# Performance work log

Hardware: AMD Instinct MI355X
Metric: run time of the kernel (lower is better)

Reference implementation:

```python
import jax, jax.numpy as jnp
import numpy as np
from jax import lax

B, C, H, W = 32, 256, 64, 64
BN_EPS = 1e-5
GRN_EPS = 1e-6


def _dwconv(x, w):
    # x: (B,C,H,W), w: (C,1,k,k) depthwise (feature_group_count=C), 'same' padding
    k = w.shape[-1]
    p = k // 2
    return lax.conv_general_dilated(
        x, w, window_strides=(1, 1), padding=[(p, p), (p, p)],
        feature_group_count=x.shape[1],
        dimension_numbers=('NCHW', 'OIHW', 'NCHW'))


def _bn(x, w, b, m, v):
    # eval-mode BatchNorm2d, per-channel affine
    scale = (w * lax.rsqrt(v + BN_EPS))[None, :, None, None]
    shift = (b - m * w * lax.rsqrt(v + BN_EPS))[None, :, None, None]
    return x * scale + shift


def setup_inputs() -> dict:
    key = jax.random.key(0)
    ks = jax.random.split(key, 6)
    ones = jnp.ones((C,), jnp.float32)
    zeros = jnp.zeros((C,), jnp.float32)
    return {
        'x': jax.random.normal(ks[0], (B, C, H, W), jnp.float32),
        'dw_w3': jax.random.normal(ks[1], (C, 1, 3, 3), jnp.float32) * 0.1,
        'bn3_w': ones, 'bn3_b': zeros, 'bn3_m': zeros, 'bn3_v': ones,
        'dw_w5': jax.random.normal(ks[2], (C, 1, 5, 5), jnp.float32) * 0.1,
        'bn5_w': ones, 'bn5_b': zeros, 'bn5_m': zeros, 'bn5_v': ones,
        'dw_w7': jax.random.normal(ks[3], (C, 1, 7, 7), jnp.float32) * 0.1,
        'bn7_w': ones, 'bn7_b': zeros, 'bn7_m': zeros, 'bn7_v': ones,
        'pw_w': jax.random.normal(ks[4], (C, C), jnp.float32) * (1.0 / np.sqrt(C)),
        'pwbn_w': ones, 'pwbn_b': zeros, 'pwbn_m': zeros, 'pwbn_v': ones,
        'grn_gamma': zeros, 'grn_beta': zeros,
    }


def reference(x, dw_w3, bn3_w, bn3_b, bn3_m, bn3_v,
              dw_w5, bn5_w, bn5_b, bn5_m, bn5_v,
              dw_w7, bn7_w, bn7_b, bn7_m, bn7_v,
              pw_w, pwbn_w, pwbn_b, pwbn_m, pwbn_v,
              grn_gamma, grn_beta):
    residual = x
    gelu = lambda t: jax.nn.gelu(t, approximate=False)  # torch nn.GELU default (erf)
    out = gelu(_bn(_dwconv(x, dw_w3), bn3_w, bn3_b, bn3_m, bn3_v))
    out = out + gelu(_bn(_dwconv(x, dw_w5), bn5_w, bn5_b, bn5_m, bn5_v))
    out = out + gelu(_bn(_dwconv(x, dw_w7), bn7_w, bn7_b, bn7_m, bn7_v))
    out = out / 3.0
    # pointwise 1x1 conv: contraction over channel dim
    out = jnp.einsum('bchw,oc->bohw', out, pw_w)
    out = _bn(out, pwbn_w, pwbn_b, pwbn_m, pwbn_v)
    # GRN: L2 norm over spatial dims per (B,C)
    Gx = jnp.sqrt(jnp.sum(out * out, axis=(2, 3), keepdims=True))  # (B,C,1,1)
    Nx = Gx / (jnp.mean(Gx, axis=1, keepdims=True) + GRN_EPS)
    out = out + grn_gamma[None, :, None, None] * (out * Nx) + grn_beta[None, :, None, None]
    out = out + residual
    return gelu(out)
```

## Files before the change

### kernel.cpp

```cpp
#include <hip/hip_runtime.h>
#include <hip/hip_bf16.h>
#include <math.h>

#define BB 32
#define CC 256
#define HH 64
#define HW 4096

typedef __attribute__((ext_vector_type(8))) short short8;
typedef __attribute__((ext_vector_type(4))) float f32x4;

__device__ __forceinline__ float gelu_erf(float x) {
    return 0.5f * x * (1.0f + erff(x * 0.70710678118654752f));
}

__global__ __launch_bounds__(256) void k_prep(const float* __restrict__ pw,
                                              __hip_bfloat16* __restrict__ pwb)
{
    const int i = blockIdx.x * 256 + threadIdx.x;
    pwb[i] = __float2bfloat16(pw[i]);
}

__global__ __launch_bounds__(256) void k_dwconv(
    const float* __restrict__ x,
    const float* __restrict__ w3,
    const float* __restrict__ bn3w, const float* __restrict__ bn3b,
    const float* __restrict__ bn3m, const float* __restrict__ bn3v,
    const float* __restrict__ w5,
    const float* __restrict__ bn5w, const float* __restrict__ bn5b,
    const float* __restrict__ bn5m, const float* __restrict__ bn5v,
    const float* __restrict__ w7,
    const float* __restrict__ bn7w, const float* __restrict__ bn7b,
    const float* __restrict__ bn7m, const float* __restrict__ bn7v,
    __hip_bfloat16* __restrict__ mid)
{
    __shared__ float sm[70 * 70];
    __shared__ float wl[83];
    __shared__ float bnp[6];
    const int tid = threadIdx.x;
    const int blk = blockIdx.x;
    const int c = blk & 255;
    const int b = blk >> 8;
    const float* xp = x + ((size_t)(b * CC + c)) * HW;

    for (int i = tid; i < 4900; i += 256) {
        int r = i / 70, q = i - r * 70;
        int h = r - 3, w = q - 3;
        float v = 0.f;
        if ((unsigned)h < 64u && (unsigned)w < 64u) v = xp[h * 64 + w];
        sm[i] = v;
    }
    if (tid < 9) wl[tid] = w3[c * 9 + tid];
    else if (tid < 34) wl[tid] = w5[c * 25 + tid - 9];
    else if (tid < 83) wl[tid] = w7[c * 49 + tid - 34];
    else if (tid == 83) {
        float s = bn3w[c] * rsqrtf(bn3v[c] + 1e-5f);
        bnp[0] = s; bnp[1] = bn3b[c] - bn3m[c] * s;
    } else if (tid == 84) {
        float s = bn5w[c] * rsqrtf(bn5v[c] + 1e-5f);
        bnp[2] = s; bnp[3] = bn5b[c] - bn5m[c] * s;
    } else if (tid == 85) {
        float s = bn7w[c] * rsqrtf(bn7v[c] + 1e-5f);
        bnp[4] = s; bnp[5] = bn7b[c] - bn7m[c] * s;
    }
    __syncthreads();

    const int ti = tid >> 4, tj = tid & 15;
    float a3[16], a5[16], a7[16];
#pragma unroll
    for (int i = 0; i < 16; ++i) { a3[i] = 0.f; a5[i] = 0.f; a7[i] = 0.f; }
    const float* w3l = wl;
    const float* w5l = wl + 9;
    const float* w7l = wl + 34;

#pragma unroll
    for (int pr = 0; pr < 10; ++pr) {
        float r[10];
        const float* srow = &sm[(ti * 4 + pr) * 70 + tj * 4];
#pragma unroll
        for (int q = 0; q < 10; ++q) r[q] = srow[q];
#pragma unroll
        for (int i = 0; i < 4; ++i) {
            const int k7 = pr - i;
            if (k7 >= 0 && k7 <= 6) {
#pragma unroll
                for (int j = 0; j < 4; ++j) {
                    float s = 0.f;
#pragma unroll
                    for (int dx = 0; dx < 7; ++dx) s += r[j + dx] * w7l[k7 * 7 + dx];
                    a7[i * 4 + j] += s;
                }
            }
            const int k5 = pr - 1 - i;
            if (k5 >= 0 && k5 <= 4) {
#pragma unroll
                for (int j = 0; j < 4; ++j) {
                    float s = 0.f;
#pragma unroll
                    for (int dx = 0; dx < 5; ++dx) s += r[j + dx + 1] * w5l[k5 * 5 + dx];
                    a5[i * 4 + j] += s;
                }
            }
            const int k3 = pr - 2 - i;
            if (k3 >= 0 && k3 <= 2) {
#pragma unroll
                for (int j = 0; j < 4; ++j) {
                    float s = 0.f;
#pragma unroll
                    for (int dx = 0; dx < 3; ++dx) s += r[j + dx + 2] * w3l[k3 * 3 + dx];
                    a3[i * 4 + j] += s;
                }
            }
        }
    }

    const float s3 = bnp[0], h3 = bnp[1], s5 = bnp[2], h5 = bnp[3], s7 = bnp[4], h7 = bnp[5];
    __hip_bfloat16* mp = mid + ((size_t)(b * CC + c)) * HW;
#pragma unroll
    for (int i = 0; i < 4; ++i) {
        __hip_bfloat16 o[4];
#pragma unroll
        for (int j = 0; j < 4; ++j) {
            float v = gelu_erf(a3[i * 4 + j] * s3 + h3)
                    + gelu_erf(a5[i * 4 + j] * s5 + h5)
                    + gelu_erf(a7[i * 4 + j] * s7 + h7);
            o[j] = __float2bfloat16(v * (1.0f / 3.0f));
        }
        *(uint2*)&mp[(ti * 4 + i) * 64 + tj * 4] = *(uint2*)o;
    }
}

#define ASTR 68
#define BSTR 40
__global__ __launch_bounds__(256) void k_pw(
    const __hip_bfloat16* __restrict__ mid,
    const __hip_bfloat16* __restrict__ pwb,
    const float* __restrict__ pbw, const float* __restrict__ pbb,
    const float* __restrict__ pbm, const float* __restrict__ pbv,
    __hip_bfloat16* __restrict__ out2,
    float* __restrict__ gx2)
{
    __shared__ __align__(16) short As[32 * ASTR];
    __shared__ __align__(16) short Bs[256 * BSTR];
    __shared__ float sc[256], sh[256], gxp[256];

    const int tid = threadIdx.x;
    const int blk = blockIdx.x;
    const int mt = blk & 63, b = blk >> 6;
    const int hw0 = mt * 64;

    {
        float s = pbw[tid] * rsqrtf(pbv[tid] + 1e-5f);
        sc[tid] = s;
        sh[tid] = pbb[tid] - pbm[tid] * s;
        gxp[tid] = 0.f;
    }

    const int wv = tid >> 6, lane = tid & 63;
    const int qd = lane >> 4, ln16 = lane & 15;

    f32x4 acc[16];
#pragma unroll
    for (int i = 0; i < 16; ++i) acc[i] = (f32x4){0.f, 0.f, 0.f, 0.f};

    const int ak = tid >> 3, am = tid & 7;
    const __hip_bfloat16* aptr = mid + ((size_t)(b * CC + ak)) * HW + hw0 + am * 8;
    const __hip_bfloat16* bptr = pwb + (size_t)tid * 256;

    for (int kk = 0; kk < 8; ++kk) {
        __syncthreads();
        uint4 av = *(const uint4*)(aptr + (size_t)kk * 32 * HW);
        *(uint2*)&As[ak * ASTR + am * 8]     = make_uint2(av.x, av.y);
        *(uint2*)&As[ak * ASTR + am * 8 + 4] = make_uint2(av.z, av.w);
        const uint4* bp = (const uint4*)(bptr + kk * 32);
#pragma unroll
        for (int j = 0; j < 4; ++j) {
            *(uint4*)&Bs[tid * BSTR + j * 8] = bp[j];
        }
        __syncthreads();

        short8 af;
        const int mloc = wv * 16 + ln16;
#pragma unroll
        for (int j = 0; j < 8; ++j) af[j] = As[(qd * 8 + j) * ASTR + mloc];
#pragma unroll
        for (int nt = 0; nt < 16; ++nt) {
            short8 bf = *(short8*)&Bs[(nt * 16 + ln16) * BSTR + qd * 8];
            acc[nt] = __builtin_amdgcn_mfma_f32_16x16x32_bf16(af, bf, acc[nt], 0, 0, 0);
        }
    }

    const size_t obase = ((size_t)b * CC) * HW + hw0 + wv * 16 + qd * 4;
#pragma unroll
    for (int nt = 0; nt < 16; ++nt) {
        const int o = nt * 16 + ln16;
        const float s = sc[o], h = sh[o];
        float v0 = acc[nt][0] * s + h;
        float v1 = acc[nt][1] * s + h;
        float v2 = acc[nt][2] * s + h;
        float v3 = acc[nt][3] * s + h;
        float p = v0 * v0 + v1 * v1 + v2 * v2 + v3 * v3;
        p += __shfl_xor(p, 16);
        p += __shfl_xor(p, 32);
        if ((lane & 48) == 0) atomicAdd(&gxp[o], p);
        __hip_bfloat16 ov[4];
        ov[0] = __float2bfloat16(v0);
        ov[1] = __float2bfloat16(v1);
        ov[2] = __float2bfloat16(v2);
        ov[3] = __float2bfloat16(v3);
        *(uint2*)&out2[obase + (size_t)o * HW] = *(uint2*)ov;
    }
    __syncthreads();
    atomicAdd(&gx2[b * CC + tid], gxp[tid]);
}

__global__ __launch_bounds__(256) void k_grn(const float* __restrict__ gx2,
                                             float* __restrict__ nx)
{
    const int b = blockIdx.x, t = threadIdx.x;
    const float g = sqrtf(gx2[b * 256 + t]);
    float s = g;
#pragma unroll
    for (int m = 1; m <= 32; m <<= 1) s += __shfl_xor(s, m);
    __shared__ float ws4[4];
    if ((t & 63) == 0) ws4[t >> 6] = s;
    __syncthreads();
    const float tot = ws4[0] + ws4[1] + ws4[2] + ws4[3];
    const float mean = tot * (1.0f / 256.0f);
    nx[b * 256 + t] = g / (mean + 1e-6f);
}

__global__ __launch_bounds__(256) void k_final(
    const __hip_bfloat16* __restrict__ out2,
    const float* __restrict__ x,
    const float* __restrict__ gamma,
    const float* __restrict__ beta,
    const float* __restrict__ nx,
    float* __restrict__ out)
{
    const size_t e = ((size_t)blockIdx.x * 256 + threadIdx.x) * 8;
    const int bc = (int)(e >> 12);
    const int c = bc & 255;
    const float m1 = 1.0f + gamma[c] * nx[bc];
    const float bt = beta[c];

    union { uint4 u; __hip_bfloat16 h[8]; } ov;
    ov.u = *(const uint4*)(out2 + e);
    float4 xa = *(const float4*)(x + e);
    float4 xb = *(const float4*)(x + e + 4);

    float4 ra, rb;
    ra.x = gelu_erf(__bfloat162float(ov.h[0]) * m1 + bt + xa.x);
    ra.y = gelu_erf(__bfloat162float(ov.h[1]) * m1 + bt + xa.y);
    ra.z = gelu_erf(__bfloat162float(ov.h[2]) * m1 + bt + xa.z);
    ra.w = gelu_erf(__bfloat162float(ov.h[3]) * m1 + bt + xa.w);
    rb.x = gelu_erf(__bfloat162float(ov.h[4]) * m1 + bt + xb.x);
    rb.y = gelu_erf(__bfloat162float(ov.h[5]) * m1 + bt + xb.y);
    rb.z = gelu_erf(__bfloat162float(ov.h[6]) * m1 + bt + xb.z);
    rb.w = gelu_erf(__bfloat162float(ov.h[7]) * m1 + bt + xb.w);

    *(float4*)(out + e) = ra;
    *(float4*)(out + e + 4) = rb;
}

extern "C" void kernel_launch(void* const* d_in, const int* in_sizes, int n_in,
                              void* d_out, int out_size, void* d_ws, size_t ws_size,
                              hipStream_t stream)
{
    const float* x    = (const float*)d_in[0];
    const float* w3   = (const float*)d_in[1];
    const float* bn3w = (const float*)d_in[2];
    const float* bn3b = (const float*)d_in[3];
    const float* bn3m = (const float*)d_in[4];
    const float* bn3v = (const float*)d_in[5];
    const float* w5   = (const float*)d_in[6];
    const float* bn5w = (const float*)d_in[7];
    const float* bn5b = (const float*)d_in[8];
    const float* bn5m = (const float*)d_in[9];
    const float* bn5v = (const float*)d_in[10];
    const float* w7   = (const float*)d_in[11];
    const float* bn7w = (const float*)d_in[12];
    const float* bn7b = (const float*)d_in[13];
    const float* bn7m = (const float*)d_in[14];
    const float* bn7v = (const float*)d_in[15];
    const float* pww  = (const float*)d_in[16];
    const float* pbw  = (const float*)d_in[17];
    const float* pbb  = (const float*)d_in[18];
    const float* pbm  = (const float*)d_in[19];
    const float* pbv  = (const float*)d_in[20];
    const float* gga  = (const float*)d_in[21];
    const float* gbe  = (const float*)d_in[22];

    char* ws = (char*)d_ws;
    const size_t nelem = (size_t)BB * CC * HW;
    __hip_bfloat16* mid  = (__hip_bfloat16*)ws;
    __hip_bfloat16* out2 = (__hip_bfloat16*)(ws + nelem * 2);
    __hip_bfloat16* pwb  = (__hip_bfloat16*)(ws + nelem * 4);
    float* gx2 = (float*)(ws + nelem * 4 + 131072);
    float* nxb = (float*)(ws + nelem * 4 + 131072 + BB * CC * sizeof(float));

    hipMemsetAsync(gx2, 0, BB * CC * sizeof(float), stream);

    k_prep<<<CC * CC / 256, 256, 0, stream>>>(pww, pwb);
    k_dwconv<<<BB * CC, 256, 0, stream>>>(x, w3, bn3w, bn3b, bn3m, bn3v,
                                          w5, bn5w, bn5b, bn5m, bn5v,
                                          w7, bn7w, bn7b, bn7m, bn7v, mid);
    k_pw<<<BB * (HW / 64), 256, 0, stream>>>(mid, pwb, pbw, pbb, pbm, pbv, out2, gx2);
    k_grn<<<BB, 256, 0, stream>>>(gx2, nxb);
    k_final<<<(int)(nelem / (256 * 8)), 256, 0, stream>>>(out2, x, gga, gbe, nxb,
                                                          (float*)d_out);
}
```

Baseline: 619.7 us.

## Rewrite depthwise conv as sliding-row register window and use tanh-approx GELU

```diff
diff --git a/kernel.cpp b/kernel.cpp
--- a/kernel.cpp
+++ b/kernel.cpp
@@ -10,8 +10,10 @@
 typedef __attribute__((ext_vector_type(8))) short short8;
 typedef __attribute__((ext_vector_type(4))) float f32x4;
 
-__device__ __forceinline__ float gelu_erf(float x) {
-    return 0.5f * x * (1.0f + erff(x * 0.70710678118654752f));
+__device__ __forceinline__ float gelu_fast(float v) {
+    float u = v * __builtin_fmaf(0.0713548162f, v * v, 1.5957691216f);
+    float e = __expf(u);
+    return v - __fdividef(v, 1.0f + e);
 }
 
 __global__ __launch_bounds__(256) void k_prep(const float* __restrict__ pw,
@@ -21,7 +23,7 @@
     pwb[i] = __float2bfloat16(pw[i]);
 }
 
-__global__ __launch_bounds__(256) void k_dwconv(
+__global__ __launch_bounds__(256, 3) void k_dwconv(
     const float* __restrict__ x,
     const float* __restrict__ w3,
     const float* __restrict__ bn3w, const float* __restrict__ bn3b,
@@ -35,13 +37,19 @@
     __hip_bfloat16* __restrict__ mid)
 {
     __shared__ float sm[70 * 70];
-    __shared__ float wl[83];
-    __shared__ float bnp[6];
+    __shared__ __align__(16) float wls[84];
     const int tid = threadIdx.x;
     const int blk = blockIdx.x;
     const int c = blk & 255;
     const int b = blk >> 8;
     const float* xp = x + ((size_t)(b * CC + c)) * HW;
+
+    const float s3 = bn3w[c] * rsqrtf(bn3v[c] + 1e-5f);
+    const float h3 = bn3b[c] - bn3m[c] * s3;
+    const float s5 = bn5w[c] * rsqrtf(bn5v[c] + 1e-5f);
+    const float h5 = bn5b[c] - bn5m[c] * s5;
+    const float s7 = bn7w[c] * rsqrtf(bn7v[c] + 1e-5f);
+    const float h7 = bn7b[c] - bn7m[c] * s7;
 
     for (int i = tid; i < 4900; i += 256) {
         int r = i / 70, q = i - r * 70;
@@ -50,83 +58,66 @@
         if ((unsigned)h < 64u && (unsigned)w < 64u) v = xp[h * 64 + w];
         sm[i] = v;
     }
-    if (tid < 9) wl[tid] = w3[c * 9 + tid];
-    else if (tid < 34) wl[tid] = w5[c * 25 + tid - 9];
-    else if (tid < 83) wl[tid] = w7[c * 49 + tid - 34];
-    else if (tid == 83) {
-        float s = bn3w[c] * rsqrtf(bn3v[c] + 1e-5f);
-        bnp[0] = s; bnp[1] = bn3b[c] - bn3m[c] * s;
-    } else if (tid == 84) {
-        float s = bn5w[c] * rsqrtf(bn5v[c] + 1e-5f);
-        bnp[2] = s; bnp[3] = bn5b[c] - bn5m[c] * s;
-    } else if (tid == 85) {
-        float s = bn7w[c] * rsqrtf(bn7v[c] + 1e-5f);
-        bnp[4] = s; bnp[5] = bn7b[c] - bn7m[c] * s;
-    }
+    if (tid < 9) wls[tid] = w3[c * 9 + tid] * s3;
+    else if (tid < 34) wls[tid] = w5[c * 25 + tid - 9] * s5;
+    else if (tid < 83) wls[tid] = w7[c * 49 + tid - 34] * s7;
+    else if (tid == 83) wls[83] = 0.f;
     __syncthreads();
 
-    const int ti = tid >> 4, tj = tid & 15;
-    float a3[16], a5[16], a7[16];
-#pragma unroll
-    for (int i = 0; i < 16; ++i) { a3[i] = 0.f; a5[i] = 0.f; a7[i] = 0.f; }
-    const float* w3l = wl;
-    const float* w5l = wl + 9;
-    const float* w7l = wl + 34;
-
-#pragma unroll
-    for (int pr = 0; pr < 10; ++pr) {
-        float r[10];
-        const float* srow = &sm[(ti * 4 + pr) * 70 + tj * 4];
-#pragma unroll
-        for (int q = 0; q < 10; ++q) r[q] = srow[q];
-#pragma unroll
-        for (int i = 0; i < 4; ++i) {
-            const int k7 = pr - i;
-            if (k7 >= 0 && k7 <= 6) {
-#pragma unroll
-                for (int j = 0; j < 4; ++j) {
-                    float s = 0.f;
-#pragma unroll
-                    for (int dx = 0; dx < 7; ++dx) s += r[j + dx] * w7l[k7 * 7 + dx];
-                    a7[i * 4 + j] += s;
-                }
-            }
-            const int k5 = pr - 1 - i;
-            if (k5 >= 0 && k5 <= 4) {
-#pragma unroll
-                for (int j = 0; j < 4; ++j) {
-                    float s = 0.f;
-#pragma unroll
-                    for (int dx = 0; dx < 5; ++dx) s += r[j + dx + 1] * w5l[k5 * 5 + dx];
-                    a5[i * 4 + j] += s;
-                }
-            }
-            const int k3 = pr - 2 - i;
-            if (k3 >= 0 && k3 <= 2) {
-#pragma unroll
-                for (int j = 0; j < 4; ++j) {
-                    float s = 0.f;
-#pragma unroll
-                    for (int dx = 0; dx < 3; ++dx) s += r[j + dx + 2] * w3l[k3 * 3 + dx];
-                    a3[i * 4 + j] += s;
-                }
-            }
-        }
-    }
-
-    const float s3 = bnp[0], h3 = bnp[1], s5 = bnp[2], h5 = bnp[3], s7 = bnp[4], h7 = bnp[5];
+    float wr[84];
+#pragma unroll
+    for (int i = 0; i < 21; ++i) {
+        float4 q = *(const float4*)&wls[i * 4];
+        wr[i * 4 + 0] = q.x; wr[i * 4 + 1] = q.y;
+        wr[i * 4 + 2] = q.z; wr[i * 4 + 3] = q.w;
+    }
+    const float* w3r = &wr[0];
+    const float* w5r = &wr[9];
+    const float* w7r = &wr[34];
+
+    const int col = tid & 63;
+    const int rg = tid >> 6;
+    const int r0 = rg * 16;
+
+    float w[7][7];
+#pragma unroll
+    for (int j = 0; j < 6; ++j) {
+        const float* srow = &sm[(r0 + j) * 70 + col];
+#pragma unroll
+        for (int d = 0; d < 7; ++d) w[j][d] = srow[d];
+    }
+
     __hip_bfloat16* mp = mid + ((size_t)(b * CC + c)) * HW;
-#pragma unroll
-    for (int i = 0; i < 4; ++i) {
-        __hip_bfloat16 o[4];
-#pragma unroll
-        for (int j = 0; j < 4; ++j) {
-            float v = gelu_erf(a3[i * 4 + j] * s3 + h3)
-                    + gelu_erf(a5[i * 4 + j] * s5 + h5)
-                    + gelu_erf(a7[i * 4 + j] * s7 + h7);
-            o[j] = __float2bfloat16(v * (1.0f / 3.0f));
-        }
-        *(uint2*)&mp[(ti * 4 + i) * 64 + tj * 4] = *(uint2*)o;
+
+#pragma unroll
+    for (int r = 0; r < 16; ++r) {
+        {
+            const float* srow = &sm[(r0 + r + 6) * 70 + col];
+            float* wd = w[(r + 6) % 7];
+#pragma unroll
+            for (int d = 0; d < 7; ++d) wd[d] = srow[d];
+        }
+        float a7 = h7, a5 = h5, a3 = h3;
+#pragma unroll
+        for (int i = 0; i < 7; ++i) {
+            const float* wrow = w[(r + i) % 7];
+#pragma unroll
+            for (int d = 0; d < 7; ++d) a7 = __builtin_fmaf(wrow[d], w7r[i * 7 + d], a7);
+        }
+#pragma unroll
+        for (int i = 1; i <= 5; ++i) {
+            const float* wrow = w[(r + i) % 7];
+#pragma unroll
+            for (int d = 1; d <= 5; ++d) a5 = __builtin_fmaf(wrow[d], w5r[(i - 1) * 5 + d - 1], a5);
+        }
+#pragma unroll
+        for (int i = 2; i <= 4; ++i) {
+            const float* wrow = w[(r + i) % 7];
+#pragma unroll
+            for (int d = 2; d <= 4; ++d) a3 = __builtin_fmaf(wrow[d], w3r[(i - 2) * 3 + d - 2], a3);
+        }
+        float v = (gelu_fast(a7) + gelu_fast(a5) + gelu_fast(a3)) * (1.0f / 3.0f);
+        mp[(r0 + r) * 64 + col] = __float2bfloat16(v);
     }
 }
 
@@ -250,14 +241,14 @@
     float4 xb = *(const float4*)(x + e + 4);
 
     float4 ra, rb;
-    ra.x = gelu_erf(__bfloat162float(ov.h[0]) * m1 + bt + xa.x);
-    ra.y = gelu_erf(__bfloat162float(ov.h[1]) * m1 + bt + xa.y);
-    ra.z = gelu_erf(__bfloat162float(ov.h[2]) * m1 + bt + xa.z);
-    ra.w = gelu_erf(__bfloat162float(ov.h[3]) * m1 + bt + xa.w);
-    rb.x = gelu_erf(__bfloat162float(ov.h[4]) * m1 + bt + xb.x);
-    rb.y = gelu_erf(__bfloat162float(ov.h[5]) * m1 + bt + xb.y);
-    rb.z = gelu_erf(__bfloat162float(ov.h[6]) * m1 + bt + xb.z);
-    rb.w = gelu_erf(__bfloat162float(ov.h[7]) * m1 + bt + xb.w);
+    ra.x = gelu_fast(__bfloat162float(ov.h[0]) * m1 + bt + xa.x);
+    ra.y = gelu_fast(__bfloat162float(ov.h[1]) * m1 + bt + xa.y);
+    ra.z = gelu_fast(__bfloat162float(ov.h[2]) * m1 + bt + xa.z);
+    ra.w = gelu_fast(__bfloat162float(ov.h[3]) * m1 + bt + xa.w);
+    rb.x = gelu_fast(__bfloat162float(ov.h[4]) * m1 + bt + xb.x);
+    rb.y = gelu_fast(__bfloat162float(ov.h[5]) * m1 + bt + xb.y);
+    rb.z = gelu_fast(__bfloat162float(ov.h[6]) * m1 + bt + xb.z);
+    rb.w = gelu_fast(__bfloat162float(ov.h[7]) * m1 + bt + xb.w);
 
     *(float4*)(out + e) = ra;
     *(float4*)(out + e + 4) = rb;
```

Result: faster. 525.0 us (-15.3%).
